# Kernel tuning notes

Hardware: AMD Instinct MI355X
Metric: run time of the kernel (lower is better)

## Reference

```python
import jax, jax.numpy as jnp
import numpy as np

NEG_SLOPE = 0.2

def gat_conv(x, src, dst, W, a_s, a_d, b, num_nodes, heads, out_c, concat):
    # x: [N, F_in]; W: [F_in, heads*out_c]; a_s/a_d: [heads, out_c]
    h = (x @ W).reshape(num_nodes, heads, out_c)          # [N,H,C]
    alpha_src = jnp.sum(h * a_s, axis=-1)                 # [N,H]
    alpha_dst = jnp.sum(h * a_d, axis=-1)                 # [N,H]
    e = jax.nn.leaky_relu(alpha_src[src] + alpha_dst[dst], NEG_SLOPE)  # [E,H]
    m = jax.ops.segment_max(e, dst, num_segments=num_nodes)           # [N,H]
    e = jnp.exp(e - m[dst])
    s = jax.ops.segment_sum(e, dst, num_segments=num_nodes)
    alpha = e / (s[dst] + 1e-16)                          # [E,H]
    out = jax.ops.segment_sum(h[src] * alpha[:, :, None], dst, num_segments=num_nodes)  # [N,H,C]
    if concat:
        out = out.reshape(num_nodes, heads * out_c)
    else:
        out = out.mean(axis=1)
    return out + b


def setup_inputs() -> dict:
    key = jax.random.key(0)
    ks = jax.random.split(key, 16)
    N, E, P = 50000, 800000, 200000
    F_in, Hd, C_out, H = 128, 32, 64, 4
    inp = {
        'x': jax.random.normal(ks[0], (N, F_in), dtype=jnp.float32),
        'edge_index': jax.random.randint(ks[1], (2, E), 0, N, dtype=jnp.int32),
        'edge_pairs': jax.random.randint(ks[2], (2, P), 0, N, dtype=jnp.int32),
        'W1': jax.random.normal(ks[3], (F_in, H * Hd), dtype=jnp.float32) * 0.05,
        'att_src1': jax.random.normal(ks[4], (H, Hd), dtype=jnp.float32) * 0.05,
        'att_dst1': jax.random.normal(ks[5], (H, Hd), dtype=jnp.float32) * 0.05,
        'b1': jnp.zeros((H * Hd,), dtype=jnp.float32),
        'W2': jax.random.normal(ks[6], (H * Hd, C_out), dtype=jnp.float32) * 0.05,
        'att_src2': jax.random.normal(ks[7], (1, C_out), dtype=jnp.float32) * 0.05,
        'att_dst2': jax.random.normal(ks[8], (1, C_out), dtype=jnp.float32) * 0.05,
        'b2': jnp.zeros((C_out,), dtype=jnp.float32),
        'Wm1': jax.random.normal(ks[9], (2 * C_out, Hd), dtype=jnp.float32) * 0.05,
        'bm1': jnp.zeros((Hd,), dtype=jnp.float32),
        'Wm2': jax.random.normal(ks[10], (Hd, 1), dtype=jnp.float32) * 0.05,
        'bm2': jnp.zeros((1,), dtype=jnp.float32),
    }
    return inp


def reference(x, edge_index, edge_pairs, W1, att_src1, att_dst1, b1,
              W2, att_src2, att_dst2, b2, Wm1, bm1, Wm2, bm2):
    N = x.shape[0]
    # add self-loops (PyG GATConv default)
    loop = jnp.arange(N, dtype=edge_index.dtype)
    src = jnp.concatenate([edge_index[0], loop])
    dst = jnp.concatenate([edge_index[1], loop])
    h = gat_conv(x, src, dst, W1, att_src1, att_dst1, b1, N, 4, 32, concat=True)
    h = jax.nn.elu(h)
    h = gat_conv(h, src, dst, W2, att_src2, att_dst2, b2, N, 1, 64, concat=True)
    ps, pd = edge_pairs[0], edge_pairs[1]
    ef = jnp.concatenate([h[ps], h[pd]], axis=-1)          # [P, 2*C_out]
    out = jax.nn.relu(ef @ Wm1 + bm1) @ Wm2 + bm2          # [P,1]
    return out[:, 0]
```

## Files before the change

### kernel.cpp

```cpp
#include <hip/hip_runtime.h>
#include <hip/hip_bf16.h>
#include <hip/hip_fp16.h>


#define LRELU_SLOPE 0.2f
#define BKT_SH 7
#define NB_MAX 512

typedef _Float16 v8h __attribute__((ext_vector_type(8)));
typedef float    v4f __attribute__((ext_vector_type(4)));

__global__ void __launch_bounds__(256) zero_prep_kernel(
    const float* __restrict__ W1, const float* __restrict__ W2,
    const float* __restrict__ Wm1,
    _Float16* __restrict__ W1Th, _Float16* __restrict__ W2Th,
    float* __restrict__ Wm1T, uint4* __restrict__ zp, int zn4)
{
    int i = blockIdx.x * 256 + threadIdx.x;
    if (i < zn4) zp[i] = make_uint4(0u, 0u, 0u, 0u);
    if (i < 16384) {
        int k = i >> 7, j = i & 127;
        W1Th[j * 128 + k] = (_Float16)W1[i];
    } else if (i < 16384 + 8192) {
        int t = i - 16384;
        int k = t >> 6, j = t & 63;
        W2Th[j * 128 + k] = (_Float16)W2[t];
    } else if (i < 16384 + 8192 + 4096) {
        int t = i - 24576;
        int k = t >> 5, j = t & 31;
        Wm1T[j * 128 + k] = Wm1[t];
    }
}

template<int AHALF>
__device__ __forceinline__ void gemm_att_body(
    int bx, int by,
    const void* __restrict__ Xv, const _Float16* __restrict__ WTH,
    const float* __restrict__ atts, const float* __restrict__ attd,
    _Float16* __restrict__ OUT, float* __restrict__ oas, float* __restrict__ oad,
    int N, int ncols, int H, int headShift)
{
    __shared__ _Float16 cs[64 * 68];
    int tid = threadIdx.x;
    int lane = tid & 63;
    int wv = tid >> 6;
    int rowBase = bx * 64 + wv * 16;
    int colBase = by * 64;
    int lr = lane & 15;
    int lk = lane >> 4;

    v8h bf[4][4];
    #pragma unroll
    for (int ct = 0; ct < 4; ct++) {
        const _Float16* bp = WTH + (size_t)(colBase + ct * 16 + lr) * 128 + lk * 8;
        #pragma unroll
        for (int ks = 0; ks < 4; ks++)
            bf[ct][ks] = *(const v8h*)(bp + ks * 32);
    }

    int arow = rowBase + lr;
    if (arow >= N) arow = N - 1;
    v4f acc[4];
    #pragma unroll
    for (int ct = 0; ct < 4; ct++) acc[ct] = (v4f){0.f, 0.f, 0.f, 0.f};

    if (AHALF) {
        const _Float16* ap = (const _Float16*)Xv + (size_t)arow * 128 + lk * 8;
        #pragma unroll
        for (int ks = 0; ks < 4; ks++) {
            v8h af = *(const v8h*)(ap + ks * 32);
            #pragma unroll
            for (int ct = 0; ct < 4; ct++)
                acc[ct] = __builtin_amdgcn_mfma_f32_16x16x32_f16(af, bf[ct][ks],
                                                                 acc[ct], 0, 0, 0);
        }
    } else {
        const float* ap = (const float*)Xv + (size_t)arow * 128 + lk * 8;
        #pragma unroll
        for (int ks = 0; ks < 4; ks++) {
            float4 a0 = *(const float4*)(ap + ks * 32);
            float4 a1 = *(const float4*)(ap + ks * 32 + 4);
            v8h af;
            af[0] = (_Float16)a0.x; af[1] = (_Float16)a0.y;
            af[2] = (_Float16)a0.z; af[3] = (_Float16)a0.w;
            af[4] = (_Float16)a1.x; af[5] = (_Float16)a1.y;
            af[6] = (_Float16)a1.z; af[7] = (_Float16)a1.w;
            #pragma unroll
            for (int ct = 0; ct < 4; ct++)
                acc[ct] = __builtin_amdgcn_mfma_f32_16x16x32_f16(af, bf[ct][ks],
                                                                 acc[ct], 0, 0, 0);
        }
    }

    int ctPerHead = (1 << headShift) >> 4;
    #pragma unroll
    for (int hh = 0; hh < 2; hh++) {
        if (hh * ctPerHead >= 4) break;
        float ps[4] = {0.f, 0.f, 0.f, 0.f};
        float pd[4] = {0.f, 0.f, 0.f, 0.f};
        for (int c2 = 0; c2 < ctPerHead; c2++) {
            int ct = hh * ctPerHead + c2;
            int col = colBase + ct * 16 + lr;
            float ws = atts[col], wd = attd[col];
            #pragma unroll
            for (int r = 0; r < 4; r++) {
                ps[r] = fmaf(acc[ct][r], ws, ps[r]);
                pd[r] = fmaf(acc[ct][r], wd, pd[r]);
            }
        }
        #pragma unroll
        for (int r = 0; r < 4; r++) {
            #pragma unroll
            for (int m = 1; m < 16; m <<= 1) {
                ps[r] += __shfl_xor(ps[r], m);
                pd[r] += __shfl_xor(pd[r], m);
            }
        }
        if (lr == 0) {
            int head = (colBase >> headShift) + hh;
            #pragma unroll
            for (int r = 0; r < 4; r++) {
                int row = rowBase + lk * 4 + r;
                if (row < N) {
                    oas[(size_t)row * H + head] = ps[r];
                    oad[(size_t)row * H + head] = pd[r];
                }
            }
        }
    }

    #pragma unroll
    for (int ct = 0; ct < 4; ct++)
        #pragma unroll
        for (int r = 0; r < 4; r++)
            cs[(wv * 16 + lk * 4 + r) * 68 + ct * 16 + lr] = (_Float16)acc[ct][r];
    __syncthreads();
    int rr = tid >> 2;
    int cb = (tid & 3) * 16;
    int grow = bx * 64 + rr;
    if (grow < N) {
        const uint4* sp = (const uint4*)(cs + rr * 68 + cb);
        _Float16* op = OUT + (size_t)grow * ncols + colBase + cb;
        uint4 w0 = sp[0];
        uint4 w1 = sp[1];
        *(uint4*)op = w0;
        *(uint4*)(op + 8) = w1;
    }
}

__device__ __forceinline__ void passA_body(
    int blk, const int* __restrict__ src, const int* __restrict__ dst,
    int E, int N, int* __restrict__ bktcnt, int* __restrict__ lbase_g, int nbkt)
{
    __shared__ int lcnt[NB_MAX];
    int tid = threadIdx.x;
    int EN = E + N;
    int base = blk * 4096;
    for (int b = tid; b < nbkt; b += 256) lcnt[b] = 0;
    __syncthreads();
    #pragma unroll
    for (int j = 0; j < 16; j++) {
        int i = base + j * 256 + tid;
        if (i < EN) {
            int d = (i < E) ? dst[i] : (i - E);
            atomicAdd(&lcnt[d >> BKT_SH], 1);
        }
    }
    __syncthreads();
    for (int b = tid; b < nbkt; b += 256) {
        int c = lcnt[b];
        lbase_g[(size_t)blk * nbkt + b] = c ? atomicAdd(&bktcnt[b], c) : 0;
    }
}

__global__ void __launch_bounds__(256) gemm1_passA_kernel(
    const float* __restrict__ X, const _Float16* __restrict__ WTH,
    const float* __restrict__ atts, const float* __restrict__ attd,
    _Float16* __restrict__ OUT, float* __restrict__ oas, float* __restrict__ oad,
    int N, int nbG,
    const int* __restrict__ src, const int* __restrict__ dst, int E,
    int* __restrict__ bktcnt, int* __restrict__ lbase_g, int nbkt)
{
    if ((int)blockIdx.x < 2 * nbG) {
        gemm_att_body<0>(blockIdx.x % nbG, blockIdx.x / nbG, X, WTH, atts, attd,
                         OUT, oas, oad, N, 128, 4, 5);
    } else {
        passA_body((int)blockIdx.x - 2 * nbG, src, dst, E, N, bktcnt, lbase_g, nbkt);
    }
}

__global__ void __launch_bounds__(256) gemm2_kernel(
    const _Float16* __restrict__ X, const _Float16* __restrict__ WTH,
    const float* __restrict__ atts, const float* __restrict__ attd,
    _Float16* __restrict__ OUT, float* __restrict__ oas, float* __restrict__ oad,
    int N)
{
    gemm_att_body<1>(blockIdx.x, 0, X, WTH, atts, attd, OUT, oas, oad,
                     N, 64, 1, 6);
}

__global__ void __launch_bounds__(512) scanb_kernel(
    const int* __restrict__ bktcnt, int* __restrict__ bktoff, int nbkt)
{
    __shared__ int wsum[8];
    int t = threadIdx.x, lane = t & 63, wid = t >> 6;
    int v = (t < nbkt) ? bktcnt[t] : 0;
    #pragma unroll
    for (int off = 1; off < 64; off <<= 1) {
        int y = __shfl_up(v, off);
        if (lane >= off) v += y;
    }
    if (lane == 63) wsum[wid] = v;
    __syncthreads();
    if (wid == 0) {
        int s = (lane < 8) ? wsum[lane] : 0;
        #pragma unroll
        for (int off = 1; off < 8; off <<= 1) {
            int y = __shfl_up(s, off);
            if (lane >= off) s += y;
        }
        if (lane < 8) wsum[lane] = s;
    }
    __syncthreads();
    if (wid > 0) v += wsum[wid - 1];
    if (t < nbkt) bktoff[t + 1] = v;
    if (t == 0) bktoff[0] = 0;
}

__global__ void __launch_bounds__(256) passB_kernel(
    const int* __restrict__ src, const int* __restrict__ dst, int E, int N,
    const int* __restrict__ bktoff, const int* __restrict__ lbase_g,
    uint2* __restrict__ ebuf, int nbkt)
{
    __shared__ int sbase[NB_MAX];
    __shared__ int loff[NB_MAX];
    int blk = blockIdx.x;
    int tid = threadIdx.x;
    int EN = E + N;
    int base = blk * 4096;
    for (int b = tid; b < nbkt; b += 256) {
        sbase[b] = bktoff[b] + lbase_g[(size_t)blk * nbkt + b];
        loff[b] = 0;
    }
    __syncthreads();
    #pragma unroll
    for (int j = 0; j < 16; j++) {
        int i = base + j * 256 + tid;
        if (i < EN) {
            int s, d;
            if (i < E) { s = src[i]; d = dst[i]; } else { s = d = i - E; }
            int b = d >> BKT_SH;
            int off = atomicAdd(&loff[b], 1);
            ebuf[(size_t)sbase[b] + off] = make_uint2((unsigned)d, (unsigned)s);
        }
    }
}

__global__ void __launch_bounds__(256) build_kernel(
    const uint2* __restrict__ ebuf, const int* __restrict__ bktoff,
    int* __restrict__ rowp, int* __restrict__ csrs, int N, int nbkt)
{
    __shared__ int ldeg[128];
    __shared__ int lrow[129];
    __shared__ int lcur[128];
    __shared__ int w0tot;
    int b = blockIdx.x;
    if (b >= nbkt) return;
    int n0 = b << BKT_SH;
    int n1 = n0 + 128; if (n1 > N) n1 = N;
    int r0 = bktoff[b], r1 = bktoff[b + 1];
    int t = threadIdx.x;
    if (t < 128) { ldeg[t] = 0; lcur[t] = 0; }
    __syncthreads();
    for (int i = r0 + t; i < r1; i += 256)
        atomicAdd(&ldeg[(int)ebuf[i].x - n0], 1);
    __syncthreads();
    int lane = t & 63;
    int v = (t < 128) ? ldeg[t] : 0;
    #pragma unroll
    for (int off = 1; off < 64; off <<= 1) {
        int y = __shfl_up(v, off);
        if (lane >= off) v += y;
    }
    if (t == 63) w0tot = v;
    __syncthreads();
    if (t >= 64 && t < 128) v += w0tot;
    if (t < 128) lrow[t + 1] = v;
    if (t == 0) { lrow[0] = 0; rowp[n0] = r0; }
    if (t < n1 - n0) rowp[n0 + t + 1] = r0 + v;
    __syncthreads();
    for (int i = r0 + t; i < r1; i += 256) {
        uint2 e = ebuf[i];
        int d = (int)e.x - n0;
        int pos = r0 + lrow[d] + atomicAdd(&lcur[d], 1);
        csrs[pos] = (int)e.y;
    }
}

template<int K>
__device__ __forceinline__ void chunk1(
    const int* __restrict__ csr, int base, int cnt,
    const float* __restrict__ as1, float adv,
    int el, int hh, int hd, int lane, const __half2* __restrict__ h1,
    float& accx, float& accy, float& srun)
{
    float wvA = 0.f, wvB = 0.f;
    if (el < cnt) {
        int s = csr[base + el];
        float e = as1[s * 4 + hh] + adv;
        e = e > 0.f ? e : LRELU_SLOPE * e;
        wvA = __expf(e);
    }
    if (K > 16 && el + 16 < cnt) {
        int s = csr[base + 16 + el];
        float e = as1[s * 4 + hh] + adv;
        e = e > 0.f ? e : LRELU_SLOPE * e;
        wvB = __expf(e);
    }
    float t = wvA + wvB;
    t += __shfl_xor(t, 4);  t += __shfl_xor(t, 8);
    t += __shfl_xor(t, 16); t += __shfl_xor(t, 32);
    srun += t;
    __half2 hv[K];
    #pragma unroll
    for (int e2 = 0; e2 < K; ++e2) {
        int ee = e2 < cnt ? e2 : cnt - 1;
        int s = csr[base + ee];
        hv[e2] = h1[(size_t)s * 64 + lane];
    }
    #pragma unroll
    for (int e2 = 0; e2 < K; ++e2) {
        float av = (e2 < 16) ? __shfl(wvA, (e2 << 2) | hd)
                             : __shfl(wvB, ((e2 - 16) << 2) | hd);
        float2 v = __half22float2(hv[e2]);
        accx = fmaf(av, v.x, accx);
        accy = fmaf(av, v.y, accy);
    }
}

__global__ void __launch_bounds__(256) edge1_kernel(
    const int* __restrict__ csr, const int* __restrict__ rowp,
    const __half2* __restrict__ h1, const float* __restrict__ as1,
    const float* __restrict__ ad1, const float* __restrict__ b1,
    __half* __restrict__ x2h, int N)
{
    int lane = threadIdx.x & 63;
    int n = __builtin_amdgcn_readfirstlane(blockIdx.x * 4 + (threadIdx.x >> 6));
    if (n >= N) return;
    int rs = rowp[n], re = rowp[n + 1];
    int hd = lane >> 4;
    int el = lane >> 2, hh = lane & 3;
    float adv = ad1[n * 4 + hh];
    float accx = 0.f, accy = 0.f, srun = 0.f;
    int base = rs, rem = re - rs;
    while (rem >= 32) {
        chunk1<32>(csr, base, 32, as1, adv, el, hh, hd, lane, h1, accx, accy, srun);
        base += 32; rem -= 32;
    }
    if (rem > 24)      chunk1<32>(csr, base, rem, as1, adv, el, hh, hd, lane, h1, accx, accy, srun);
    else if (rem > 16) chunk1<24>(csr, base, rem, as1, adv, el, hh, hd, lane, h1, accx, accy, srun);
    else if (rem > 8)  chunk1<16>(csr, base, rem, as1, adv, el, hh, hd, lane, h1, accx, accy, srun);
    else if (rem > 0)  chunk1<8> (csr, base, rem, as1, adv, el, hh, hd, lane, h1, accx, accy, srun);

    float sden = __shfl(srun, hd) + 1e-16f;
    float inv = 1.f / sden;
    float2 bv = *(const float2*)(b1 + lane * 2);
    float o0 = accx * inv + bv.x;
    float o1 = accy * inv + bv.y;
    o0 = o0 > 0.f ? o0 : (__expf(o0) - 1.f);
    o1 = o1 > 0.f ? o1 : (__expf(o1) - 1.f);
    *(__half2*)(x2h + (size_t)n * 128 + lane * 2) = __floats2half2_rn(o0, o1);
}

template<int K>
__device__ __forceinline__ void chunk2(
    const int* __restrict__ csr, int base, int cnt,
    const float* __restrict__ as2, float adv, int lane,
    const __half* __restrict__ h2, float& acc, float& srun)
{
    float wv = 0.f;
    if (lane < cnt) {
        int s = csr[base + lane];
        float e = as2[s] + adv;
        e = e > 0.f ? e : LRELU_SLOPE * e;
        wv = __expf(e);
    }
    srun += wv;
    __half hv[K];
    #pragma unroll
    for (int e2 = 0; e2 < K; ++e2) {
        int ee = e2 < cnt ? e2 : cnt - 1;
        int s = csr[base + ee];
        hv[e2] = h2[(size_t)s * 64 + lane];
    }
    #pragma unroll
    for (int e2 = 0; e2 < K; ++e2) {
        float av = __shfl(wv, e2);
        acc = fmaf(av, __half2float(hv[e2]), acc);
    }
}

__global__ void __launch_bounds__(256) edge2_kernel(
    const int* __restrict__ csr, const int* __restrict__ rowp,
    const __half* __restrict__ h2, const float* __restrict__ as2,
    const float* __restrict__ ad2, const float* __restrict__ b2,
    float* __restrict__ hf, int N)
{
    int lane = threadIdx.x & 63;
    int n = __builtin_amdgcn_readfirstlane(blockIdx.x * 4 + (threadIdx.x >> 6));
    if (n >= N) return;
    int rs = rowp[n], re = rowp[n + 1];
    float adv = ad2[n];
    float acc = 0.f, srun = 0.f;
    int base = rs, rem = re - rs;
    while (rem >= 16) {
        chunk2<16>(csr, base, 16, as2, adv, lane, h2, acc, srun);
        base += 16; rem -= 16;
    }
    if (rem > 8)      chunk2<16>(csr, base, rem, as2, adv, lane, h2, acc, srun);
    else if (rem > 0) chunk2<8> (csr, base, rem, as2, adv, lane, h2, acc, srun);

    #pragma unroll
    for (int m = 1; m < 64; m <<= 1) srun += __shfl_xor(srun, m);
    float o = acc / (srun + 1e-16f) + b2[lane];
    hf[(size_t)n * 64 + lane] = o;
}

__global__ void __launch_bounds__(256) node_mlp_kernel(
    const float* __restrict__ hf, const float* __restrict__ Wm1T,
    __half* __restrict__ uv, int N)
{
    int lane = threadIdx.x & 63;
    int j = lane & 31, half = lane >> 5;
    const float* wr = Wm1T + j * 128 + half * 64;
    float wreg[64];
    #pragma unroll
    for (int q = 0; q < 16; q++) {
        float4 t = ((const float4*)wr)[q];
        wreg[q*4] = t.x; wreg[q*4+1] = t.y; wreg[q*4+2] = t.z; wreg[q*4+3] = t.w;
    }
    int wgid = __builtin_amdgcn_readfirstlane(blockIdx.x * 4 + (threadIdx.x >> 6));
    int nwaves = gridDim.x * 4;
    for (int n = wgid; n < N; n += nwaves) {
        const float* hr = hf + (size_t)n * 64;
        float acc = 0.f;
        #pragma unroll
        for (int k = 0; k < 64; k += 4) {
            float4 hv = *(const float4*)(hr + k);
            acc = fmaf(hv.x, wreg[k],   acc);
            acc = fmaf(hv.y, wreg[k+1], acc);
            acc = fmaf(hv.z, wreg[k+2], acc);
            acc = fmaf(hv.w, wreg[k+3], acc);
        }
        uv[(size_t)n * 64 + lane] = __float2half_rn(acc);
    }
}

__global__ void __launch_bounds__(256) pair_mlp_kernel(
    const int* __restrict__ ps, const int* __restrict__ pd,
    const __half2* __restrict__ uv, const float* __restrict__ bm1,
    const float* __restrict__ Wm2, const float* __restrict__ bm2,
    float* __restrict__ out, int P)
{
    int gid = blockIdx.x * 256 + threadIdx.x;
    int p = gid >> 1;
    if (p >= P) return;
    int half = gid & 1;
    int j0 = half * 8;
    int a = ps[p], b = pd[p];
    const __half2* ua = uv + (size_t)a * 32 + j0;
    const __half2* vb = uv + (size_t)b * 32 + 16 + j0;
    float r = 0.f;
    #pragma unroll
    for (int q = 0; q < 8; q++) {
        float2 uu = __half22float2(ua[q]);
        float2 vv = __half22float2(vb[q]);
        float2 bb = *(const float2*)(bm1 + half * 16 + q * 2);
        float2 ww = *(const float2*)(Wm2 + half * 16 + q * 2);
        float h0 = uu.x + vv.x + bb.x; h0 = h0 > 0.f ? h0 : 0.f; r = fmaf(h0, ww.x, r);
        float h1 = uu.y + vv.y + bb.y; h1 = h1 > 0.f ? h1 : 0.f; r = fmaf(h1, ww.y, r);
    }
    r += __shfl_xor(r, 1);
    if (half == 0) out[p] = r + bm2[0];
}

extern "C" void kernel_launch(void* const* d_in, const int* in_sizes, int n_in,
                              void* d_out, int out_size, void* d_ws, size_t ws_size,
                              hipStream_t stream)
{
    const float* x    = (const float*)d_in[0];
    const int*   ei   = (const int*)  d_in[1];
    const int*   ep   = (const int*)  d_in[2];
    const float* W1   = (const float*)d_in[3];
    const float* atS1 = (const float*)d_in[4];
    const float* atD1 = (const float*)d_in[5];
    const float* b1   = (const float*)d_in[6];
    const float* W2   = (const float*)d_in[7];
    const float* atS2 = (const float*)d_in[8];
    const float* atD2 = (const float*)d_in[9];
    const float* b2   = (const float*)d_in[10];
    const float* Wm1  = (const float*)d_in[11];
    const float* bm1  = (const float*)d_in[12];
    const float* Wm2  = (const float*)d_in[13];
    const float* bm2  = (const float*)d_in[14];
    float* out = (float*)d_out;

    int N = in_sizes[0] / 128;
    int E = in_sizes[1] / 2;
    int P = in_sizes[2] / 2;
    int Etot = E + N;
    int EN = Etot;
    int nbkt = (N + (1 << BKT_SH) - 1) >> BKT_SH;
    int nbA  = (EN + 4095) / 4096;

    char* w = (char*)d_ws;
    auto alloc = [&](size_t bytes) {
        char* p = w; w += (bytes + 255) & ~(size_t)255; return p;
    };
    _Float16* W1Th = (_Float16*)alloc(16384 * 2);
    _Float16* W2Th = (_Float16*)alloc(8192 * 2);
    float*    Wm1T = (float*)alloc(4096 * 4);
    _Float16* h1   = (_Float16*)alloc((size_t)N * 128 * 2);
    __half*   x2h  = (__half*)alloc((size_t)N * 128 * 2);
    _Float16* h2   = (_Float16*)alloc((size_t)N * 64 * 2);
    float*    hf   = (float*)alloc((size_t)N * 64 * 4);
    int*      rowp = (int*)alloc((size_t)(N + 1) * 4);
    int*      bktoff = (int*)alloc((size_t)(nbkt + 1) * 4);
    int*      csrs = (int*)alloc((size_t)Etot * 4);
    uint2*    ebuf = (uint2*)alloc((size_t)Etot * 8);
    int*      lbase_g = (int*)alloc((size_t)nbA * nbkt * 4);
    char* z0 = w;
    int*   bktcnt = (int*)alloc(NB_MAX * 4);
    char* z1 = w;
    float* as1  = (float*)alloc((size_t)N * 4 * 4);
    float* ad1  = (float*)alloc((size_t)N * 4 * 4);
    float* as2  = (float*)alloc((size_t)N * 4);
    float* ad2  = (float*)alloc((size_t)N * 4);
    __half* uv = (__half*)alloc((size_t)N * 64 * 2);

    int zn4 = (int)((z1 - z0) / 16);
    zero_prep_kernel<<<112, 256, 0, stream>>>(W1, W2, Wm1, W1Th, W2Th, Wm1T,
                                              (uint4*)z0, zn4);

    int nbG = (N + 63) / 64;
    gemm1_passA_kernel<<<2 * nbG + nbA, 256, 0, stream>>>(
        x, W1Th, atS1, atD1, h1, as1, ad1, N, nbG,
        ei, ei + E, E, bktcnt, lbase_g, nbkt);

    scanb_kernel<<<1, 512, 0, stream>>>(bktcnt, bktoff, nbkt);
    passB_kernel<<<nbA, 256, 0, stream>>>(ei, ei + E, E, N, bktoff, lbase_g,
                                          ebuf, nbkt);
    build_kernel<<<nbkt, 256, 0, stream>>>(ebuf, bktoff, rowp, csrs, N, nbkt);

    edge1_kernel<<<(N + 3) / 4, 256, 0, stream>>>(csrs, rowp, (const __half2*)h1,
                                                  as1, ad1, b1, x2h, N);
    gemm2_kernel<<<nbG, 256, 0, stream>>>((const _Float16*)x2h, W2Th, atS2, atD2,
                                          h2, as2, ad2, N);
    edge2_kernel<<<(N + 3) / 4, 256, 0, stream>>>(csrs, rowp, (const __half*)h2,
                                                  as2, ad2, b2, hf, N);

    node_mlp_kernel<<<1024, 256, 0, stream>>>(hf, Wm1T, uv, N);
    pair_mlp_kernel<<<(2 * P + 255) / 256, 256, 0, stream>>>(ep, ep + P,
                                                             (const __half2*)uv,
                                                             bm1, Wm2, bm2, out, P);
}
```

Measured before the change: 169.3 us.

## Fuse node MLP into edge2 and replace atomic bucket bases with deterministic scan

The per-node MLP projection now runs inside the layer-2 edge aggregation kernel. Each wave stages its output row in shared memory and dots it with the Wm1T rows, which removes the fp32 hf buffer round trip and one launch. The bucket sort no longer uses global atomics for per-block bases: passA writes raw per-block counts and a single-block scan kernel serially prefix-sums them per bucket. That drops the zeroing work in the prep kernel, but the scan now loops over all blocks serially, roughly 200 iterations per thread, and each edge2 wave re-reads Wm1T.

```diff
diff --git a/kernel.cpp b/kernel.cpp
--- a/kernel.cpp
+++ b/kernel.cpp
@@ -10,14 +10,13 @@
 typedef _Float16 v8h __attribute__((ext_vector_type(8)));
 typedef float    v4f __attribute__((ext_vector_type(4)));
 
-__global__ void __launch_bounds__(256) zero_prep_kernel(
+__global__ void __launch_bounds__(256) prep_kernel(
     const float* __restrict__ W1, const float* __restrict__ W2,
     const float* __restrict__ Wm1,
     _Float16* __restrict__ W1Th, _Float16* __restrict__ W2Th,
-    float* __restrict__ Wm1T, uint4* __restrict__ zp, int zn4)
+    float* __restrict__ Wm1T)
 {
     int i = blockIdx.x * 256 + threadIdx.x;
-    if (i < zn4) zp[i] = make_uint4(0u, 0u, 0u, 0u);
     if (i < 16384) {
         int k = i >> 7, j = i & 127;
         W1Th[j * 128 + k] = (_Float16)W1[i];
@@ -150,7 +149,7 @@
 
 __device__ __forceinline__ void passA_body(
     int blk, const int* __restrict__ src, const int* __restrict__ dst,
-    int E, int N, int* __restrict__ bktcnt, int* __restrict__ lbase_g, int nbkt)
+    int E, int N, int* __restrict__ lcnt_g, int nbkt)
 {
     __shared__ int lcnt[NB_MAX];
     int tid = threadIdx.x;
@@ -167,10 +166,8 @@
         }
     }
     __syncthreads();
-    for (int b = tid; b < nbkt; b += 256) {
-        int c = lcnt[b];
-        lbase_g[(size_t)blk * nbkt + b] = c ? atomicAdd(&bktcnt[b], c) : 0;
-    }
+    for (int b = tid; b < nbkt; b += 256)
+        lcnt_g[(size_t)blk * nbkt + b] = lcnt[b];
 }
 
 __global__ void __launch_bounds__(256) gemm1_passA_kernel(
@@ -179,13 +176,13 @@
     _Float16* __restrict__ OUT, float* __restrict__ oas, float* __restrict__ oad,
     int N, int nbG,
     const int* __restrict__ src, const int* __restrict__ dst, int E,
-    int* __restrict__ bktcnt, int* __restrict__ lbase_g, int nbkt)
+    int* __restrict__ lcnt_g, int nbkt)
 {
     if ((int)blockIdx.x < 2 * nbG) {
         gemm_att_body<0>(blockIdx.x % nbG, blockIdx.x / nbG, X, WTH, atts, attd,
                          OUT, oas, oad, N, 128, 4, 5);
     } else {
-        passA_body((int)blockIdx.x - 2 * nbG, src, dst, E, N, bktcnt, lbase_g, nbkt);
+        passA_body((int)blockIdx.x - 2 * nbG, src, dst, E, N, lcnt_g, nbkt);
     }
 }
 
@@ -199,12 +196,22 @@
                      N, 64, 1, 6);
 }
 
-__global__ void __launch_bounds__(512) scanb_kernel(
-    const int* __restrict__ bktcnt, int* __restrict__ bktoff, int nbkt)
+__global__ void __launch_bounds__(512) scanb2_kernel(
+    int* __restrict__ lcnt_g, int* __restrict__ bktoff, int nbkt, int nbA)
 {
     __shared__ int wsum[8];
-    int t = threadIdx.x, lane = t & 63, wid = t >> 6;
-    int v = (t < nbkt) ? bktcnt[t] : 0;
+    int t = threadIdx.x;
+    int cum = 0;
+    if (t < nbkt) {
+        for (int blk = 0; blk < nbA; ++blk) {
+            size_t idx = (size_t)blk * nbkt + t;
+            int v = lcnt_g[idx];
+            lcnt_g[idx] = cum;
+            cum += v;
+        }
+    }
+    int lane = t & 63, wid = t >> 6;
+    int v = (t < nbkt) ? cum : 0;
     #pragma unroll
     for (int off = 1; off < 64; off <<= 1) {
         int y = __shfl_up(v, off);
@@ -229,7 +236,7 @@
 
 __global__ void __launch_bounds__(256) passB_kernel(
     const int* __restrict__ src, const int* __restrict__ dst, int E, int N,
-    const int* __restrict__ bktoff, const int* __restrict__ lbase_g,
+    const int* __restrict__ bktoff, const int* __restrict__ lcnt_g,
     uint2* __restrict__ ebuf, int nbkt)
 {
     __shared__ int sbase[NB_MAX];
@@ -239,7 +246,7 @@
     int EN = E + N;
     int base = blk * 4096;
     for (int b = tid; b < nbkt; b += 256) {
-        sbase[b] = bktoff[b] + lbase_g[(size_t)blk * nbkt + b];
+        sbase[b] = bktoff[b] + lcnt_g[(size_t)blk * nbkt + b];
         loff[b] = 0;
     }
     __syncthreads();
@@ -400,14 +407,16 @@
     }
 }
 
-__global__ void __launch_bounds__(256) edge2_kernel(
+__global__ void __launch_bounds__(256) edge2_mlp_kernel(
     const int* __restrict__ csr, const int* __restrict__ rowp,
     const __half* __restrict__ h2, const float* __restrict__ as2,
     const float* __restrict__ ad2, const float* __restrict__ b2,
-    float* __restrict__ hf, int N)
-{
+    const float* __restrict__ Wm1T, __half* __restrict__ uv, int N)
+{
+    __shared__ float ols[4][64];
     int lane = threadIdx.x & 63;
-    int n = __builtin_amdgcn_readfirstlane(blockIdx.x * 4 + (threadIdx.x >> 6));
+    int wvid = threadIdx.x >> 6;
+    int n = __builtin_amdgcn_readfirstlane(blockIdx.x * 4 + wvid);
     if (n >= N) return;
     int rs = rowp[n], re = rowp[n + 1];
     float adv = ad2[n];
@@ -423,37 +432,21 @@
     #pragma unroll
     for (int m = 1; m < 64; m <<= 1) srun += __shfl_xor(srun, m);
     float o = acc / (srun + 1e-16f) + b2[lane];
-    hf[(size_t)n * 64 + lane] = o;
-}
-
-__global__ void __launch_bounds__(256) node_mlp_kernel(
-    const float* __restrict__ hf, const float* __restrict__ Wm1T,
-    __half* __restrict__ uv, int N)
-{
-    int lane = threadIdx.x & 63;
+    ols[wvid][lane] = o;
+
     int j = lane & 31, half = lane >> 5;
     const float* wr = Wm1T + j * 128 + half * 64;
-    float wreg[64];
+    float dot = 0.f;
     #pragma unroll
     for (int q = 0; q < 16; q++) {
-        float4 t = ((const float4*)wr)[q];
-        wreg[q*4] = t.x; wreg[q*4+1] = t.y; wreg[q*4+2] = t.z; wreg[q*4+3] = t.w;
-    }
-    int wgid = __builtin_amdgcn_readfirstlane(blockIdx.x * 4 + (threadIdx.x >> 6));
-    int nwaves = gridDim.x * 4;
-    for (int n = wgid; n < N; n += nwaves) {
-        const float* hr = hf + (size_t)n * 64;
-        float acc = 0.f;
-        #pragma unroll
-        for (int k = 0; k < 64; k += 4) {
-            float4 hv = *(const float4*)(hr + k);
-            acc = fmaf(hv.x, wreg[k],   acc);
-            acc = fmaf(hv.y, wreg[k+1], acc);
-            acc = fmaf(hv.z, wreg[k+2], acc);
-            acc = fmaf(hv.w, wreg[k+3], acc);
-        }
-        uv[(size_t)n * 64 + lane] = __float2half_rn(acc);
-    }
+        float4 wv4 = ((const float4*)wr)[q];
+        float4 hv4 = *(const float4*)&ols[wvid][q * 4];
+        dot = fmaf(hv4.x, wv4.x, dot);
+        dot = fmaf(hv4.y, wv4.y, dot);
+        dot = fmaf(hv4.z, wv4.z, dot);
+        dot = fmaf(hv4.w, wv4.w, dot);
+    }
+    uv[(size_t)n * 64 + lane] = __float2half_rn(dot);
 }
 
 __global__ void __launch_bounds__(256) pair_mlp_kernel(
@@ -523,32 +516,26 @@
     _Float16* h1   = (_Float16*)alloc((size_t)N * 128 * 2);
     __half*   x2h  = (__half*)alloc((size_t)N * 128 * 2);
     _Float16* h2   = (_Float16*)alloc((size_t)N * 64 * 2);
-    float*    hf   = (float*)alloc((size_t)N * 64 * 4);
     int*      rowp = (int*)alloc((size_t)(N + 1) * 4);
     int*      bktoff = (int*)alloc((size_t)(nbkt + 1) * 4);
     int*      csrs = (int*)alloc((size_t)Etot * 4);
     uint2*    ebuf = (uint2*)alloc((size_t)Etot * 8);
-    int*      lbase_g = (int*)alloc((size_t)nbA * nbkt * 4);
-    char* z0 = w;
-    int*   bktcnt = (int*)alloc(NB_MAX * 4);
-    char* z1 = w;
-    float* as1  = (float*)alloc((size_t)N * 4 * 4);
-    float* ad1  = (float*)alloc((size_t)N * 4 * 4);
-    float* as2  = (float*)alloc((size_t)N * 4);
-    float* ad2  = (float*)alloc((size_t)N * 4);
-    __half* uv = (__half*)alloc((size_t)N * 64 * 2);
-
-    int zn4 = (int)((z1 - z0) / 16);
-    zero_prep_kernel<<<112, 256, 0, stream>>>(W1, W2, Wm1, W1Th, W2Th, Wm1T,
-                                              (uint4*)z0, zn4);
+    int*      lcnt_g = (int*)alloc((size_t)nbA * nbkt * 4);
+    float*    as1  = (float*)alloc((size_t)N * 4 * 4);
+    float*    ad1  = (float*)alloc((size_t)N * 4 * 4);
+    float*    as2  = (float*)alloc((size_t)N * 4);
+    float*    ad2  = (float*)alloc((size_t)N * 4);
+    __half*   uv   = (__half*)alloc((size_t)N * 64 * 2);
+
+    prep_kernel<<<112, 256, 0, stream>>>(W1, W2, Wm1, W1Th, W2Th, Wm1T);
 
     int nbG = (N + 63) / 64;
     gemm1_passA_kernel<<<2 * nbG + nbA, 256, 0, stream>>>(
         x, W1Th, atS1, atD1, h1, as1, ad1, N, nbG,
-        ei, ei + E, E, bktcnt, lbase_g, nbkt);
-
-    scanb_kernel<<<1, 512, 0, stream>>>(bktcnt, bktoff, nbkt);
-    passB_kernel<<<nbA, 256, 0, stream>>>(ei, ei + E, E, N, bktoff, lbase_g,
+        ei, ei + E, E, lcnt_g, nbkt);
+
+    scanb2_kernel<<<1, 512, 0, stream>>>(lcnt_g, bktoff, nbkt, nbA);
+    passB_kernel<<<nbA, 256, 0, stream>>>(ei, ei + E, E, N, bktoff, lcnt_g,
                                           ebuf, nbkt);
     build_kernel<<<nbkt, 256, 0, stream>>>(ebuf, bktoff, rowp, csrs, N, nbkt);
 
@@ -556,10 +543,10 @@
                                                   as1, ad1, b1, x2h, N);
     gemm2_kernel<<<nbG, 256, 0, stream>>>((const _Float16*)x2h, W2Th, atS2, atD2,
                                           h2, as2, ad2, N);
-    edge2_kernel<<<(N + 3) / 4, 256, 0, stream>>>(csrs, rowp, (const __half*)h2,
-                                                  as2, ad2, b2, hf, N);
-
-    node_mlp_kernel<<<1024, 256, 0, stream>>>(hf, Wm1T, uv, N);
+    edge2_mlp_kernel<<<(N + 3) / 4, 256, 0, stream>>>(csrs, rowp,
+                                                      (const __half*)h2,
+                                                      as2, ad2, b2, Wm1T, uv, N);
+
     pair_mlp_kernel<<<(2 * P + 255) / 256, 256, 0, stream>>>(ep, ep + P,
                                                              (const __half2*)uv,
                                                              bm1, Wm2, bm2, out, P);
```

Result: slower. 261.3 us (+54.4%).
